# Kernel tuning notes

Measured on AMD Instinct MI355X. Metric: run time of the kernel, lower is better.

## Reference

```python
import jax, jax.numpy as jnp
import numpy as np

N_NODES = 100000
N_EDGES = 3200000


def setup_inputs() -> dict:
    key = jax.random.key(0)
    ks = jax.random.split(key, 12)
    x = jax.random.normal(ks[0], (N_NODES, 5), dtype=jnp.float32)
    edges = jax.random.randint(ks[1], (2, N_EDGES), 0, N_NODES)
    edge_attr = jax.random.normal(ks[2], (N_EDGES, 2), dtype=jnp.float32)
    detector_labels = jax.random.bernoulli(ks[3], 0.7, (N_NODES,))

    def init(k, shape, fan_in):
        return (jax.random.normal(k, shape, dtype=jnp.float32) / np.sqrt(fan_in)).astype(jnp.float32)

    W_gat = init(ks[4], (5, 16), 5)        # GATConv lin (shared src/dst)
    att_src = init(ks[5], (16,), 16)
    att_dst = init(ks[6], (16,), 16)
    W_edge = init(ks[7], (2, 16), 2)       # GATConv lin_edge
    att_edge = init(ks[8], (16,), 16)
    b_gat = jnp.zeros((16,), jnp.float32)
    W1 = init(ks[9], (34, 64), 34)
    b1 = jnp.zeros((64,), jnp.float32)
    W2 = init(ks[10], (64, 2), 64)
    b2 = jnp.zeros((2,), jnp.float32)
    return dict(x=x, edges=edges, edge_attr=edge_attr, detector_labels=detector_labels,
                W_gat=W_gat, att_src=att_src, att_dst=att_dst, W_edge=W_edge,
                att_edge=att_edge, b_gat=b_gat, W1=W1, b1=b1, W2=W2, b2=b2)


def reference(x, edges, edge_attr, detector_labels, W_gat, att_src, att_dst,
              W_edge, att_edge, b_gat, W1, b1, W2, b2):
    n_nodes = x.shape[0]
    src, dst = edges[0], edges[1]

    # --- GATConv(5 -> 16, heads=1, concat=False, edge_dim=2, no self loops) ---
    h = x @ W_gat                                        # [N, 16]
    a_src = h @ att_src                                  # [N]
    a_dst = h @ att_dst                                  # [N]
    a_edge = (edge_attr @ W_edge) @ att_edge             # [E]
    alpha = jax.nn.leaky_relu(a_src[src] + a_dst[dst] + a_edge, 0.2)
    # segmented softmax over incoming edges of each dst node
    seg_max = jax.ops.segment_max(alpha, dst, num_segments=n_nodes)
    ex = jnp.exp(alpha - seg_max[dst])
    denom = jax.ops.segment_sum(ex, dst, num_segments=n_nodes)
    a = ex / (denom[dst] + 1e-16)                        # [E]
    out = jax.ops.segment_sum(h[src] * a[:, None], dst, num_segments=n_nodes) + b_gat
    xh = jax.nn.relu(out)                                # [N, 16]

    # --- edge update: gather-concat-MLP ---
    feat = jnp.concatenate([xh[src], edge_attr, xh[dst]], axis=-1)   # [E, 34]
    ef = jax.nn.relu(feat @ W1 + b1) @ W2 + b2                       # [E, 2]

    # --- SplitSyndromes: keep edges whose both endpoints are detectors ---
    valid = detector_labels[src] & detector_labels[dst]
    idx = jnp.nonzero(valid)[0]        # eager (data-dependent size, not jitted)
    return edges[:, idx], jax.nn.sigmoid(ef[idx])
```

## Files before the change

kernel.cpp:

```cpp
#include <hip/hip_runtime.h>

#define NN 100000
#define NE 3200000
#define CH 2048
#define NCB ((NE + CH - 1) / CH)
#define ITER (CH / 256)
#define NBK ((NN + 63) >> 6)
#define CAP 2560
#define NWG (NE / 64)
#define NSTRIP 8
#define SLEN ((NCB + NSTRIP - 1) / NSTRIP)

typedef __attribute__((ext_vector_type(8))) __bf16 bf16x8;
typedef __attribute__((ext_vector_type(4))) float f32x4;

union BF8 { unsigned short u[8]; bf16x8 v; };

__global__ void kdetect(const unsigned char* __restrict__ lab8, int* __restrict__ flags) {
  __shared__ int tmp[256];
  int t = threadIdx.x;
  int s = 0;
  for (int i = t; i < 25000; i += 256) s += lab8[4 * i + 1];
  tmp[t] = s;
  __syncthreads();
  for (int d = 128; d > 0; d >>= 1) { if (t < d) tmp[t] += tmp[t + d]; __syncthreads(); }
  if (t == 0) flags[0] = (tmp[0] != 0) ? 1 : 0;
}

__global__ void klab(const void* __restrict__ lab, const int* __restrict__ flags,
                     int* __restrict__ labN) {
  int n = blockIdx.x * 256 + threadIdx.x;
  if (n >= NN) return;
  int v;
  if (flags[0]) v = ((const unsigned char*)lab)[n];
  else          v = ((const int*)lab)[n];
  labN[n] = (v != 0) ? 1 : 0;
}

__global__ void kc01(const float* __restrict__ We, const float* __restrict__ ae,
                     float* __restrict__ c01) {
  if (threadIdx.x == 0) {
    float c0 = 0.f, c1 = 0.f;
    for (int k = 0; k < 16; k++) { c0 += We[k] * ae[k]; c1 += We[16 + k] * ae[k]; }
    c01[0] = c0; c01[1] = c1;
  }
}

__global__ void knodeA(const float* __restrict__ x, const float* __restrict__ Wg,
                       const float* __restrict__ atts, const float* __restrict__ attd,
                       const int* __restrict__ labN,
                       float2* __restrict__ pka, float2* __restrict__ pkd) {
  int n = blockIdx.x * 256 + threadIdx.x;
  if (n >= NN) return;
  float xi[5];
#pragma unroll
  for (int i = 0; i < 5; i++) xi[i] = x[n * 5 + i];
  float asum = 0.f, dsum = 0.f;
#pragma unroll
  for (int k = 0; k < 16; k++) {
    float acc = 0.f;
#pragma unroll
    for (int i = 0; i < 5; i++) acc += xi[i] * Wg[i * 16 + k];
    asum += acc * atts[k];
    dsum += acc * attd[k];
  }
  float lab = labN[n] ? 1.f : 0.f;
  pka[n] = make_float2(asum, lab);
  pkd[n] = make_float2(dsum, lab);
}

__global__ __launch_bounds__(256) void khist(const int* __restrict__ src,
                                             const int* __restrict__ dst,
                                             const int* __restrict__ labN,
                                             int* __restrict__ blkcnt,
                                             int* __restrict__ cntw,
                                             int* __restrict__ cntc) {
  __shared__ int hist[NBK];
  __shared__ int vsum;
  int tid = threadIdx.x, b = blockIdx.x;
  for (int i = tid; i < NBK; i += 256) hist[i] = 0;
  if (tid == 0) vsum = 0;
  __syncthreads();
  int lane = tid & 63, wid = tid >> 6;
  int wsum = 0;
  for (int it = 0; it < ITER; ++it) {
    int e = b * CH + it * 256 + tid;
    int v = 0;
    if (e < NE) {
      int s = src[e], d = dst[e];
      atomicAdd(&hist[d >> 6], 1);
      v = labN[s] & labN[d];
    }
    unsigned long long m = __ballot(v != 0);
    int c = __popcll(m);
    if (lane == 0) {
      int wg = b * (CH / 64) + it * 4 + wid;
      if (wg < NWG) cntw[wg] = c;
      wsum += c;
    }
  }
  if (lane == 0) atomicAdd(&vsum, wsum);
  __syncthreads();
  int* row = blkcnt + (size_t)b * NBK;
  for (int i = tid; i < NBK; i += 256) row[i] = hist[i];
  if (tid == 0) cntc[b] = vsum;
}

__global__ __launch_bounds__(256) void kscanc1(int* __restrict__ blkcnt,
                                               int* __restrict__ ssum) {
  int i = blockIdx.x * 256 + threadIdx.x;
  int st = blockIdx.y;
  if (i >= NBK) return;
  int c0 = st * SLEN, c1 = min(c0 + SLEN, NCB);
  int run = 0;
#pragma unroll 4
  for (int c = c0; c < c1; c++) {
    int* p = blkcnt + (size_t)c * NBK + i;
    int v = *p;
    *p = run;
    run += v;
  }
  ssum[st * NBK + i] = run;
}

__global__ __launch_bounds__(256) void kscanc2(int* __restrict__ ssum,
                                               int* __restrict__ total) {
  int i = blockIdx.x * 256 + threadIdx.x;
  if (i >= NBK) return;
  int run = 0;
#pragma unroll
  for (int st = 0; st < NSTRIP; st++) {
    int v = ssum[st * NBK + i];
    ssum[st * NBK + i] = run;
    run += v;
  }
  total[i] = run;
}

__global__ void kscan(const int* __restrict__ cnt, int* __restrict__ off, int nb) {
  __shared__ int tmp[256];
  __shared__ int carry;
  int t = threadIdx.x;
  if (t == 0) carry = 0;
  __syncthreads();
  for (int base = 0; base < nb; base += 256) {
    int i = base + t;
    int v = (i < nb) ? cnt[i] : 0;
    tmp[t] = v;
    __syncthreads();
    for (int d = 1; d < 256; d <<= 1) {
      int add = (t >= d) ? tmp[t - d] : 0;
      __syncthreads();
      tmp[t] += add;
      __syncthreads();
    }
    if (i < nb) off[i] = carry + tmp[t] - v;
    __syncthreads();
    if (t == 0) carry += tmp[255];
    __syncthreads();
  }
  if (t == 0) off[nb] = carry;
}

__global__ __launch_bounds__(128) void kscanw(const int* __restrict__ cntw,
                                              const int* __restrict__ offc,
                                              int* __restrict__ offw) {
  __shared__ int a[128];
  int t = threadIdx.x;
  int wg = blockIdx.x * 128 + t;
  int l = t & 31;
  int val = (wg < NWG) ? cntw[wg] : 0;
  a[t] = val;
  __syncthreads();
  for (int d = 1; d < 32; d <<= 1) {
    int x = (l >= d) ? a[t - d] : 0;
    __syncthreads();
    a[t] += x;
    __syncthreads();
  }
  if (wg < NWG) offw[wg] = offc[wg >> 5] + a[t] - val;
}

__global__ __launch_bounds__(256) void kscat(
    const int* __restrict__ src, const int* __restrict__ dst,
    const float* __restrict__ eattr,
    const float2* __restrict__ pka, const float2* __restrict__ pkd,
    const float* __restrict__ c01, const int* __restrict__ bucket_base,
    const int* __restrict__ blkcnt, const int* __restrict__ ssum,
    const int* __restrict__ offw,
    uint2* __restrict__ bins, float* __restrict__ out,
    float2* __restrict__ eat2, int NV) {
  __shared__ int cur[NBK];
  int ob = blockIdx.x, tid = threadIdx.x;
  int xcd = ob & 7, loc = ob >> 3;
  const int q = NCB >> 3, r = NCB & 7;
  int b = ((xcd < r) ? xcd * (q + 1) : r * (q + 1) + (xcd - r) * q) + loc;
  const int* bc = blkcnt + (size_t)b * NBK;
  const int* ss = ssum + (size_t)(b / SLEN) * NBK;
  for (int i = tid; i < NBK; i += 256) cur[i] = bucket_base[i] + ss[i] + bc[i];
  float c0 = c01[0], c1 = c01[1];
  __syncthreads();
  int lane = tid & 63, wid = tid >> 6;
  for (int it = 0; it < ITER; ++it) {
    int e = b * CH + it * 256 + tid;
    if (e >= NE) break;
    int s = src[e], d = dst[e];
    float2 ea = ((const float2*)eattr)[e];
    float2 ga = pka[s], gd = pkd[d];
    float al = ga.x + gd.x + ea.x * c0 + ea.y * c1;
    al = (al > 0.f) ? al : 0.2f * al;
    float exv = __expf(al);
    int pos = atomicAdd(&cur[d >> 6], 1);
    uint2 pl;
    pl.x = ((unsigned)s << 6) | (unsigned)(d & 63);
    pl.y = __float_as_uint(exv);
    bins[pos] = pl;
    int v = (ga.y != 0.f) && (gd.y != 0.f);
    unsigned long long m = __ballot(v);
    if (v) {
      int wg = b * (CH / 64) + it * 4 + wid;
      int p = offw[wg] + __popcll(m & ((1ull << lane) - 1ull));
      if (p < NV) {
        out[p] = (float)s;
        out[NV + p] = (float)d;
        eat2[p] = ea;
      }
    }
  }
}

__global__ __launch_bounds__(512) void kagg(
    const uint2* __restrict__ bins, const int* __restrict__ bucket_base,
    const float* __restrict__ x, const float* __restrict__ Wg,
    const float* __restrict__ bg, float* __restrict__ xh) {
  __shared__ uint2 pay[CAP];
  __shared__ int cnt[64], inc[64], cur[64];
  __shared__ float sWg[80], sbg[16];
  int k = blockIdx.x, tid = threadIdx.x;
  if (tid < 80) sWg[tid] = Wg[tid];
  else if (tid < 96) sbg[tid - 80] = bg[tid - 80];
  int start = bucket_base[k], end = bucket_base[k + 1];
  int node0 = k << 6;
  int c = tid & 15, g = tid >> 4;
  __syncthreads();
  float w0 = sWg[c], w1 = sWg[16 + c], w2 = sWg[32 + c], w3 = sWg[48 + c], w4 = sWg[64 + c];
  float acc[2] = {0.f, 0.f}, den[2] = {0.f, 0.f};
  for (int cb = start; cb < end; cb += CAP) {
    int n = min(end - cb, CAP);
    if (tid < 64) cnt[tid] = 0;
    __syncthreads();
    uint2 st0, st1, st2, st3, st4;
    {
      int i;
      i = tid;          if (i < n) { st0 = bins[cb + i]; atomicAdd(&cnt[st0.x & 63], 1); }
      i = tid + 512;    if (i < n) { st1 = bins[cb + i]; atomicAdd(&cnt[st1.x & 63], 1); }
      i = tid + 1024;   if (i < n) { st2 = bins[cb + i]; atomicAdd(&cnt[st2.x & 63], 1); }
      i = tid + 1536;   if (i < n) { st3 = bins[cb + i]; atomicAdd(&cnt[st3.x & 63], 1); }
      i = tid + 2048;   if (i < n) { st4 = bins[cb + i]; atomicAdd(&cnt[st4.x & 63], 1); }
    }
    __syncthreads();
    if (tid < 64) inc[tid] = cnt[tid];
    __syncthreads();
    for (int d = 1; d < 64; d <<= 1) {
      int v = 0;
      if (tid >= d && tid < 64) v = inc[tid - d];
      __syncthreads();
      if (tid < 64) inc[tid] += v;
      __syncthreads();
    }
    if (tid < 64) cur[tid] = inc[tid] - cnt[tid];
    __syncthreads();
    {
      int i;
      i = tid;          if (i < n) pay[atomicAdd(&cur[st0.x & 63], 1)] = st0;
      i = tid + 512;    if (i < n) pay[atomicAdd(&cur[st1.x & 63], 1)] = st1;
      i = tid + 1024;   if (i < n) pay[atomicAdd(&cur[st2.x & 63], 1)] = st2;
      i = tid + 1536;   if (i < n) pay[atomicAdd(&cur[st3.x & 63], 1)] = st3;
      i = tid + 2048;   if (i < n) pay[atomicAdd(&cur[st4.x & 63], 1)] = st4;
    }
    __syncthreads();
#pragma unroll
    for (int p = 0; p < 2; ++p) {
      int nd = p * 32 + g;
      int re = inc[nd], rs = re - cnt[nd];
      float a = 0.f, ds = 0.f;
      for (int idx = rs; idx < re; ++idx) {
        uint2 pl = pay[idx];
        int s = (int)(pl.x >> 6);
        float exv = __uint_as_float(pl.y);
        const float* xp = x + s * 5;
        float h = xp[0] * w0 + xp[1] * w1 + xp[2] * w2 + xp[3] * w3 + xp[4] * w4;
        a += h * exv;
        ds += exv;
      }
      acc[p] += a; den[p] += ds;
    }
    __syncthreads();
  }
#pragma unroll
  for (int p = 0; p < 2; ++p) {
    int node = node0 + p * 32 + g;
    if (node < NN) {
      float dn = fmaxf(den[p], 1e-30f);
      float v = acc[p] / dn + sbg[c];
      xh[node * 16 + c] = (v > 0.f) ? v : 0.f;
    }
  }
}

__global__ __launch_bounds__(256) void kmlp(
    const float2* __restrict__ eat2, const float* __restrict__ xh,
    const float* __restrict__ W1, const float* __restrict__ b1,
    const float* __restrict__ W2, const float* __restrict__ b2,
    float* __restrict__ out, int NV) {
  int tid = threadIdx.x;
  int lane = tid & 63, wid = tid >> 6;
  int lo4 = lane & 15, q = lane >> 4;

  BF8 bh[4], bl[4];
#pragma unroll
  for (int ct = 0; ct < 4; ct++) {
    int col = ct * 16 + lo4;
#pragma unroll
    for (int i = 0; i < 8; i++) {
      int k = q * 8 + i;
      int r = (k < 16) ? k : (k + 2);
      float w = W1[r * 64 + col];
      unsigned u = __float_as_uint(w);
      float rem = w - __uint_as_float(u & 0xffff0000u);
      bh[ct].u[i] = (unsigned short)(u >> 16);
      bl[ct].u[i] = (unsigned short)(__float_as_uint(rem) >> 16);
    }
  }
  float b1v[4], w16v[4], w17v[4], w2a[4], w2b[4];
#pragma unroll
  for (int ct = 0; ct < 4; ct++) {
    int j = ct * 16 + lo4;
    b1v[ct] = b1[j];
    w16v[ct] = W1[16 * 64 + j];
    w17v[ct] = W1[17 * 64 + j];
    w2a[ct] = W2[j * 2 + 0];
    w2b[ct] = W2[j * 2 + 1];
  }
  float bias20 = b2[0], bias21 = b2[1];

  int nwaves = gridDim.x * 4;
  int ntiles = (NV + 15) >> 4;
  for (int tb = blockIdx.x * 4 + wid; tb < ntiles; tb += nwaves) {
    int base = tb * 16;
    BF8 ah, al;
    {
      int p = base + lo4;
      float vals[8] = {0.f, 0.f, 0.f, 0.f, 0.f, 0.f, 0.f, 0.f};
      if (p < NV) {
        int node = (int)out[((q < 2) ? 0 : NV) + p];
        const float4* xp = (const float4*)(xh + node * 16 + (q & 1) * 8);
        float4 f0 = xp[0], f1 = xp[1];
        vals[0] = f0.x; vals[1] = f0.y; vals[2] = f0.z; vals[3] = f0.w;
        vals[4] = f1.x; vals[5] = f1.y; vals[6] = f1.z; vals[7] = f1.w;
      }
#pragma unroll
      for (int i = 0; i < 8; i++) {
        unsigned u = __float_as_uint(vals[i]);
        float rem = vals[i] - __uint_as_float(u & 0xffff0000u);
        ah.u[i] = (unsigned short)(u >> 16);
        al.u[i] = (unsigned short)(__float_as_uint(rem) >> 16);
      }
    }
    f32x4 acc[4];
#pragma unroll
    for (int ct = 0; ct < 4; ct++) {
      f32x4 z = {0.f, 0.f, 0.f, 0.f};
      z = __builtin_amdgcn_mfma_f32_16x16x32_bf16(ah.v, bh[ct].v, z, 0, 0, 0);
      z = __builtin_amdgcn_mfma_f32_16x16x32_bf16(ah.v, bl[ct].v, z, 0, 0, 0);
      z = __builtin_amdgcn_mfma_f32_16x16x32_bf16(al.v, bh[ct].v, z, 0, 0, 0);
      acc[ct] = z;
    }
    float o0[4], o1[4];
#pragma unroll
    for (int reg = 0; reg < 4; reg++) {
      int pr = base + q * 4 + reg;
      float2 ea = make_float2(0.f, 0.f);
      if (pr < NV) ea = eat2[pr];
      float s0 = 0.f, s1 = 0.f;
#pragma unroll
      for (int ct = 0; ct < 4; ct++) {
        float h = acc[ct][reg] + b1v[ct] + ea.x * w16v[ct] + ea.y * w17v[ct];
        h = fmaxf(h, 0.f);
        s0 += h * w2a[ct];
        s1 += h * w2b[ct];
      }
      o0[reg] = s0; o1[reg] = s1;
    }
#pragma unroll
    for (int m = 1; m < 16; m <<= 1) {
#pragma unroll
      for (int reg = 0; reg < 4; reg++) {
        o0[reg] += __shfl_xor(o0[reg], m, 64);
        o1[reg] += __shfl_xor(o1[reg], m, 64);
      }
    }
    if (lo4 == 0) {
#pragma unroll
      for (int reg = 0; reg < 4; reg++) {
        int pr = base + q * 4 + reg;
        if (pr < NV) {
          float v0 = bias20 + o0[reg], v1 = bias21 + o1[reg];
          ((float2*)(out + 2 * (size_t)NV))[pr] = make_float2(
              1.f / (1.f + __expf(-v0)), 1.f / (1.f + __expf(-v1)));
        }
      }
    }
  }
}

static inline size_t al64(size_t v) { return (v + 63) & ~(size_t)63; }

extern "C" void kernel_launch(void* const* d_in, const int* in_sizes, int n_in,
                              void* d_out, int out_size, void* d_ws, size_t ws_size,
                              hipStream_t stream) {
  const float* x     = (const float*)d_in[0];
  const int*   edges = (const int*)d_in[1];
  const float* eattr = (const float*)d_in[2];
  const void*  labels= d_in[3];
  const float* Wg    = (const float*)d_in[4];
  const float* atts  = (const float*)d_in[5];
  const float* attd  = (const float*)d_in[6];
  const float* We    = (const float*)d_in[7];
  const float* atte  = (const float*)d_in[8];
  const float* bg    = (const float*)d_in[9];
  const float* W1    = (const float*)d_in[10];
  const float* b1    = (const float*)d_in[11];
  const float* W2    = (const float*)d_in[12];
  const float* b2    = (const float*)d_in[13];
  float* out = (float*)d_out;
  const int NV = out_size / 4;
  const int* src = edges;
  const int* dst = edges + NE;

  char* w = (char*)d_ws;
  float* xh    = (float*)w;   w += al64((size_t)NN * 64);
  uint2* bins  = (uint2*)w;   w += al64((size_t)NE * 8);
  float2* eat2 = (float2*)w;  w += al64((size_t)NV * 8);
  float2* pka  = (float2*)w;  w += al64((size_t)NN * 8);
  float2* pkd  = (float2*)w;  w += al64((size_t)NN * 8);
  int* labN    = (int*)w;     w += al64((size_t)NN * 4);
  int* blkcnt  = (int*)w;     w += al64((size_t)NCB * NBK * 4);
  int* ssum    = (int*)w;     w += al64((size_t)NSTRIP * NBK * 4);
  int* total   = (int*)w;     w += al64((size_t)NBK * 4);
  int* bb      = (int*)w;     w += al64((size_t)(NBK + 1) * 4);
  int* cntc    = (int*)w;     w += al64((size_t)NCB * 4);
  int* offc    = (int*)w;     w += al64((size_t)(NCB + 1) * 4);
  int* cntw    = (int*)w;     w += al64((size_t)NWG * 4);
  int* offw    = (int*)w;     w += al64((size_t)NWG * 4);
  float* c01   = (float*)w;   w += 64;
  int* flags   = (int*)w;     w += 64;

  kdetect<<<1, 256, 0, stream>>>((const unsigned char*)labels, flags);
  klab<<<(NN + 255) / 256, 256, 0, stream>>>(labels, flags, labN);
  kc01<<<1, 64, 0, stream>>>(We, atte, c01);
  knodeA<<<(NN + 255) / 256, 256, 0, stream>>>(x, Wg, atts, attd, labN, pka, pkd);
  khist<<<NCB, 256, 0, stream>>>(src, dst, labN, blkcnt, cntw, cntc);
  kscanc1<<<dim3((NBK + 255) / 256, NSTRIP), 256, 0, stream>>>(blkcnt, ssum);
  kscanc2<<<(NBK + 255) / 256, 256, 0, stream>>>(ssum, total);
  kscan<<<1, 256, 0, stream>>>(total, bb, NBK);
  kscan<<<1, 256, 0, stream>>>(cntc, offc, NCB);
  kscanw<<<(NWG + 127) / 128, 128, 0, stream>>>(cntw, offc, offw);
  kscat<<<NCB, 256, 0, stream>>>(src, dst, eattr, pka, pkd, c01, bb, blkcnt, ssum,
                                 offw, bins, out, eat2, NV);
  kagg<<<NBK, 512, 0, stream>>>(bins, bb, x, Wg, bg, xh);
  if (NV > 0)
    kmlp<<<2048, 256, 0, stream>>>(eat2, xh, W1, b1, W2, b2, out, NV);
}
```

Baseline: 294.2 us.

## Enlarge edge chunks to 8192 with 1024-thread blocks and fold bucket base into strip sums

Raises the edge chunk size from 2048 to 8192 and the block size of the histogram and scatter kernels to 1024 threads. This cuts the per-chunk bucket-count matrix by four, so the column scans read and write less and the histogram and scatter kernels each initialise shared bucket counters once per larger chunk. A new small kernel adds the bucket base offsets into the strip sums ahead of time, which removes one global load per bucket in the scatter prologue. The word-offset scan is reorganised to one block per chunk of 128 warps, and the scatter loop is unrolled when the chunk is full. In exchange there are fewer blocks, so there may be less parallelism and more shared-atomic contention within each block.

```diff
diff --git a/kernel.cpp b/kernel.cpp
--- a/kernel.cpp
+++ b/kernel.cpp
@@ -2,9 +2,10 @@
 
 #define NN 100000
 #define NE 3200000
-#define CH 2048
+#define CH 8192
 #define NCB ((NE + CH - 1) / CH)
-#define ITER (CH / 256)
+#define THR 1024
+#define ITH (CH / THR)
 #define NBK ((NN + 63) >> 6)
 #define CAP 2560
 #define NWG (NE / 64)
@@ -69,7 +70,7 @@
   pkd[n] = make_float2(dsum, lab);
 }
 
-__global__ __launch_bounds__(256) void khist(const int* __restrict__ src,
+__global__ __launch_bounds__(THR) void khist(const int* __restrict__ src,
                                              const int* __restrict__ dst,
                                              const int* __restrict__ labN,
                                              int* __restrict__ blkcnt,
@@ -78,13 +79,13 @@
   __shared__ int hist[NBK];
   __shared__ int vsum;
   int tid = threadIdx.x, b = blockIdx.x;
-  for (int i = tid; i < NBK; i += 256) hist[i] = 0;
+  for (int i = tid; i < NBK; i += THR) hist[i] = 0;
   if (tid == 0) vsum = 0;
   __syncthreads();
   int lane = tid & 63, wid = tid >> 6;
   int wsum = 0;
-  for (int it = 0; it < ITER; ++it) {
-    int e = b * CH + it * 256 + tid;
+  for (int it = 0; it < ITH; ++it) {
+    int e = b * CH + it * THR + tid;
     int v = 0;
     if (e < NE) {
       int s = src[e], d = dst[e];
@@ -94,7 +95,7 @@
     unsigned long long m = __ballot(v != 0);
     int c = __popcll(m);
     if (lane == 0) {
-      int wg = b * (CH / 64) + it * 4 + wid;
+      int wg = b * (CH / 64) + it * 16 + wid;
       if (wg < NWG) cntw[wg] = c;
       wsum += c;
     }
@@ -102,7 +103,7 @@
   if (lane == 0) atomicAdd(&vsum, wsum);
   __syncthreads();
   int* row = blkcnt + (size_t)b * NBK;
-  for (int i = tid; i < NBK; i += 256) row[i] = hist[i];
+  for (int i = tid; i < NBK; i += THR) row[i] = hist[i];
   if (tid == 0) cntc[b] = vsum;
 }
 
@@ -113,7 +114,6 @@
   if (i >= NBK) return;
   int c0 = st * SLEN, c1 = min(c0 + SLEN, NCB);
   int run = 0;
-#pragma unroll 4
   for (int c = c0; c < c1; c++) {
     int* p = blkcnt + (size_t)c * NBK + i;
     int v = *p;
@@ -137,6 +137,15 @@
   total[i] = run;
 }
 
+__global__ __launch_bounds__(256) void kaddbb(int* __restrict__ ssum,
+                                              const int* __restrict__ bb) {
+  int i = blockIdx.x * 256 + threadIdx.x;
+  if (i >= NBK) return;
+  int v = bb[i];
+#pragma unroll
+  for (int st = 0; st < NSTRIP; st++) ssum[st * NBK + i] += v;
+}
+
 __global__ void kscan(const int* __restrict__ cnt, int* __restrict__ off, int nb) {
   __shared__ int tmp[256];
   __shared__ int carry;
@@ -165,27 +174,58 @@
 __global__ __launch_bounds__(128) void kscanw(const int* __restrict__ cntw,
                                               const int* __restrict__ offc,
                                               int* __restrict__ offw) {
+  int b = blockIdx.x, t = threadIdx.x;
   __shared__ int a[128];
-  int t = threadIdx.x;
-  int wg = blockIdx.x * 128 + t;
-  int l = t & 31;
+  int wg = b * 128 + t;
   int val = (wg < NWG) ? cntw[wg] : 0;
   a[t] = val;
   __syncthreads();
-  for (int d = 1; d < 32; d <<= 1) {
-    int x = (l >= d) ? a[t - d] : 0;
+  for (int d = 1; d < 128; d <<= 1) {
+    int x = (t >= d) ? a[t - d] : 0;
     __syncthreads();
     a[t] += x;
     __syncthreads();
   }
-  if (wg < NWG) offw[wg] = offc[wg >> 5] + a[t] - val;
-}
-
-__global__ __launch_bounds__(256) void kscat(
+  if (wg < NWG) offw[wg] = offc[b] + a[t] - val;
+}
+
+__device__ __forceinline__ void scat_body(
+    int e, int b, int it, int lane, int wid,
     const int* __restrict__ src, const int* __restrict__ dst,
     const float* __restrict__ eattr,
     const float2* __restrict__ pka, const float2* __restrict__ pkd,
-    const float* __restrict__ c01, const int* __restrict__ bucket_base,
+    float c0, float c1, int* cur, const int* __restrict__ offw,
+    uint2* __restrict__ bins, float* __restrict__ out,
+    float2* __restrict__ eat2, int NV) {
+  int s = src[e], d = dst[e];
+  float2 ea = ((const float2*)eattr)[e];
+  float2 ga = pka[s], gd = pkd[d];
+  float al = ga.x + gd.x + ea.x * c0 + ea.y * c1;
+  al = (al > 0.f) ? al : 0.2f * al;
+  float exv = __expf(al);
+  int pos = atomicAdd(&cur[d >> 6], 1);
+  uint2 pl;
+  pl.x = ((unsigned)s << 6) | (unsigned)(d & 63);
+  pl.y = __float_as_uint(exv);
+  bins[pos] = pl;
+  int v = (ga.y != 0.f) && (gd.y != 0.f);
+  unsigned long long m = __ballot(v);
+  if (v) {
+    int wg = b * (CH / 64) + it * 16 + wid;
+    int p = offw[wg] + __popcll(m & ((1ull << lane) - 1ull));
+    if (p < NV) {
+      out[p] = (float)s;
+      out[NV + p] = (float)d;
+      eat2[p] = ea;
+    }
+  }
+}
+
+__global__ __launch_bounds__(THR) void kscat(
+    const int* __restrict__ src, const int* __restrict__ dst,
+    const float* __restrict__ eattr,
+    const float2* __restrict__ pka, const float2* __restrict__ pkd,
+    const float* __restrict__ c01,
     const int* __restrict__ blkcnt, const int* __restrict__ ssum,
     const int* __restrict__ offw,
     uint2* __restrict__ bins, float* __restrict__ out,
@@ -197,34 +237,21 @@
   int b = ((xcd < r) ? xcd * (q + 1) : r * (q + 1) + (xcd - r) * q) + loc;
   const int* bc = blkcnt + (size_t)b * NBK;
   const int* ss = ssum + (size_t)(b / SLEN) * NBK;
-  for (int i = tid; i < NBK; i += 256) cur[i] = bucket_base[i] + ss[i] + bc[i];
+  for (int i = tid; i < NBK; i += THR) cur[i] = ss[i] + bc[i];
   float c0 = c01[0], c1 = c01[1];
   __syncthreads();
   int lane = tid & 63, wid = tid >> 6;
-  for (int it = 0; it < ITER; ++it) {
-    int e = b * CH + it * 256 + tid;
-    if (e >= NE) break;
-    int s = src[e], d = dst[e];
-    float2 ea = ((const float2*)eattr)[e];
-    float2 ga = pka[s], gd = pkd[d];
-    float al = ga.x + gd.x + ea.x * c0 + ea.y * c1;
-    al = (al > 0.f) ? al : 0.2f * al;
-    float exv = __expf(al);
-    int pos = atomicAdd(&cur[d >> 6], 1);
-    uint2 pl;
-    pl.x = ((unsigned)s << 6) | (unsigned)(d & 63);
-    pl.y = __float_as_uint(exv);
-    bins[pos] = pl;
-    int v = (ga.y != 0.f) && (gd.y != 0.f);
-    unsigned long long m = __ballot(v);
-    if (v) {
-      int wg = b * (CH / 64) + it * 4 + wid;
-      int p = offw[wg] + __popcll(m & ((1ull << lane) - 1ull));
-      if (p < NV) {
-        out[p] = (float)s;
-        out[NV + p] = (float)d;
-        eat2[p] = ea;
-      }
+  if (b * CH + CH <= NE) {
+#pragma unroll
+    for (int it = 0; it < ITH; ++it)
+      scat_body(b * CH + it * THR + tid, b, it, lane, wid, src, dst, eattr,
+                pka, pkd, c0, c1, cur, offw, bins, out, eat2, NV);
+  } else {
+    for (int it = 0; it < ITH; ++it) {
+      int e = b * CH + it * THR + tid;
+      if (e >= NE) break;
+      scat_body(e, b, it, lane, wid, src, dst, eattr,
+                pka, pkd, c0, c1, cur, offw, bins, out, eat2, NV);
     }
   }
 }
@@ -460,13 +487,14 @@
   klab<<<(NN + 255) / 256, 256, 0, stream>>>(labels, flags, labN);
   kc01<<<1, 64, 0, stream>>>(We, atte, c01);
   knodeA<<<(NN + 255) / 256, 256, 0, stream>>>(x, Wg, atts, attd, labN, pka, pkd);
-  khist<<<NCB, 256, 0, stream>>>(src, dst, labN, blkcnt, cntw, cntc);
+  khist<<<NCB, THR, 0, stream>>>(src, dst, labN, blkcnt, cntw, cntc);
   kscanc1<<<dim3((NBK + 255) / 256, NSTRIP), 256, 0, stream>>>(blkcnt, ssum);
   kscanc2<<<(NBK + 255) / 256, 256, 0, stream>>>(ssum, total);
   kscan<<<1, 256, 0, stream>>>(total, bb, NBK);
+  kaddbb<<<(NBK + 255) / 256, 256, 0, stream>>>(ssum, bb);
   kscan<<<1, 256, 0, stream>>>(cntc, offc, NCB);
-  kscanw<<<(NWG + 127) / 128, 128, 0, stream>>>(cntw, offc, offw);
-  kscat<<<NCB, 256, 0, stream>>>(src, dst, eattr, pka, pkd, c01, bb, blkcnt, ssum,
+  kscanw<<<NCB, 128, 0, stream>>>(cntw, offc, offw);
+  kscat<<<NCB, THR, 0, stream>>>(src, dst, eattr, pka, pkd, c01, blkcnt, ssum,
                                  offw, bins, out, eat2, NV);
   kagg<<<NBK, 512, 0, stream>>>(bins, bb, x, Wg, bg, xh);
   if (NV > 0)
```

Measured after the change: 290.8 us. Within noise of the previous version (-1.2%).
